# Performance work log

Hardware: AMD Instinct MI355X
Metric: run time of the kernel (lower is better)

## Reference

```python
import jax, jax.numpy as jnp
import numpy as np

K = 20          # neighbors per point
BN_EPS = 1e-5


def setup_inputs() -> dict:
    key = jax.random.key(0)
    k0, k1, k2 = jax.random.split(key, 3)
    B, N, C_OUT, EDGE_DIM = 8, 4096, 64, 4  # edge feat = [diff(3), ||diff||(1)]
    x = jax.random.normal(k0, (B, N, 3), dtype=jnp.float32)
    pos = jax.random.uniform(k1, (B, N, 3), dtype=jnp.float32)
    # shared 1x1-conv MLP params (Conv1d k=1 == per-edge linear) + BatchNorm affine
    W = jax.random.normal(k2, (C_OUT, EDGE_DIM), dtype=jnp.float32) * 0.1
    b = jnp.zeros((C_OUT,), jnp.float32)
    gamma = jnp.ones((C_OUT,), jnp.float32)
    beta = jnp.zeros((C_OUT,), jnp.float32)
    return {"x": x, "pos": pos, "W": W, "b": b, "gamma": gamma, "beta": beta}


def _knn_idx(pos, k):
    # pos: [B, N, 3] -> idx of k nearest neighbors per point, self excluded. [B, N, k]
    B, N, _ = pos.shape
    sq = jnp.sum(pos * pos, axis=-1)                                   # [B, N]
    d2 = sq[:, :, None] + sq[:, None, :] - 2.0 * jnp.einsum('bnd,bmd->bnm', pos, pos)
    d2 = d2 + jnp.eye(N, dtype=pos.dtype) * 1e10                       # exclude self-loop
    _, idx = jax.lax.top_k(-d2, k)                                     # [B, N, k]
    return idx


def _forward(pos, W, b, gamma, beta, k=K):
    idx = _knn_idx(pos, k)                                             # [B, N, k] (int, non-diff)
    nbr = jax.vmap(lambda p, i: p[i])(pos, idx)                        # gather: [B, N, k, 3]
    diff = nbr - pos[:, :, None, :]                                    # neighbor - center
    dist = jnp.sqrt(jnp.sum(diff * diff, axis=-1, keepdims=True))      # [B, N, k, 1]
    feat = jnp.concatenate([diff, dist], axis=-1)                      # [B, N, k, 4]
    # shared MLP (1x1 conv): per-edge linear
    y = jnp.einsum('bnkc,oc->bnko', feat, W) + b                       # [B, N, k, 64]
    # BatchNorm1d over all edges (training-mode batch stats), per channel
    mu = jnp.mean(y, axis=(0, 1, 2))
    var = jnp.var(y, axis=(0, 1, 2))
    y = (y - mu) * jax.lax.rsqrt(var + BN_EPS) * gamma + beta
    y = jax.nn.relu(y)
    y = jnp.where(y >= 0, y, 0.1 * y)   # leaky_relu(0.1) from source (no-op after relu, kept for fidelity)
    return jnp.mean(y, axis=2)          # mean pool over each node's k edges -> [B, N, 64]


def reference(x, pos, W, b, gamma, beta):
    # x only provides (batch_size, num_points) in the source; math uses pos.
    return _forward(pos, W, b, gamma, beta)
```

## Files before the change

kernel.cpp:

```cpp
#include <hip/hip_runtime.h>

#define NB    8
#define NP    4096
#define KNN   20
#define COUT  64
#define S     4
#define BLK   256
#define QPB   (BLK / S)
#define BPB   (NP / QPB)
#define NBLK1 (NB * BPB)
#define NBLK2 ((NB * NP * 4) / BLK)
#define NMOM  14
#define MSTR  16
#define LCAP  32
#define FBIG  3.402823466e38f

typedef unsigned long long u64;
typedef unsigned int u32;

__device__ __forceinline__ void ins20(float d, u32 mi,
                                      float* __restrict__ bd,
                                      u32* __restrict__ bi) {
#pragma unroll
    for (int j = KNN - 1; j >= 1; --j) {
        const bool sh  = d < bd[j - 1];
        const bool in_ = !sh && (d < bd[j]);
        bi[j] = sh ? bi[j - 1] : (in_ ? mi : bi[j]);
        bd[j] = fminf(fmaxf(bd[j - 1], d), bd[j]);
    }
    if (d < bd[0]) { bi[0] = mi; bd[0] = d; }
}

__global__ __launch_bounds__(BLK, 2)
void knn_kernel(const float* __restrict__ pos,
                unsigned short* __restrict__ idx_out,
                float* __restrict__ mom) {
    __shared__ float4 sp[NP];

    const int b = blockIdx.x / BPB;
    const int t = threadIdx.x;
    const int s = t & (S - 1);
    const int n = (blockIdx.x % BPB) * QPB + (t >> 2);
    const float* pb = pos + (size_t)b * NP * 3;

    for (int i = t; i < NP; i += BLK) {
        const float x = pb[3 * i], y = pb[3 * i + 1], z = pb[3 * i + 2];
        const float csq = __fadd_rn(
            __fadd_rn(__fmul_rn(x, x), __fmul_rn(y, y)), __fmul_rn(z, z));
        sp[i] = make_float4(x, y, z, csq);
    }
    __syncthreads();

    const float4 q = sp[n];

    float sd0 = FBIG, sd1 = FBIG, sd2 = FBIG, sd3 = FBIG, sd4 = FBIG;
#pragma unroll 4
    for (int i = 0; i < NP / S; i += 4) {
        const int m = (i << 2) | s;
        const float4 c = sp[m];
        const float dot = fmaf(q.z, c.z, fmaf(q.y, c.y, __fmul_rn(q.x, c.x)));
        const float d2  = __fsub_rn(__fadd_rn(q.w, c.w), __fmul_rn(2.0f, dot));
        if (m != n && d2 < sd4) {
            sd4 = fminf(fmaxf(sd3, d2), sd4);
            sd3 = fminf(fmaxf(sd2, d2), sd3);
            sd2 = fminf(fmaxf(sd1, d2), sd2);
            sd1 = fminf(fmaxf(sd0, d2), sd1);
            sd0 = fminf(sd0, d2);
        }
    }
    float gb = sd4;
    gb = fmaxf(gb, __shfl_xor(gb, 1));
    gb = fmaxf(gb, __shfl_xor(gb, 2));

    float bd[KNN];
    u32   bi[KNN];
#pragma unroll
    for (int j = 0; j < KNN; ++j) { bd[j] = FBIG; bi[j] = 0xFFFu; }
    float p0d = 0.f, p1d = 0.f, p2d = 0.f, p3d = 0.f;
    u32   p0i = 0, p1i = 0, p2i = 0, p3i = 0;
    int   cnt = 0;

#pragma unroll 2
    for (int i = 0; i < NP / S; ++i) {
        const int m = (i << 2) | s;
        const float4 c = sp[m];
        const float dot = fmaf(q.z, c.z, fmaf(q.y, c.y, __fmul_rn(q.x, c.x)));
        const float d2  = __fsub_rn(__fadd_rn(q.w, c.w), __fmul_rn(2.0f, dot));
        const bool acc = (m != n) && (d2 <= gb);
        const bool a0 = acc && (cnt == 0), a1 = acc && (cnt == 1);
        const bool a2 = acc && (cnt == 2), a3 = acc && (cnt == 3);
        p0d = a0 ? d2 : p0d;  p0i = a0 ? (u32)m : p0i;
        p1d = a1 ? d2 : p1d;  p1i = a1 ? (u32)m : p1i;
        p2d = a2 ? d2 : p2d;  p2i = a2 ? (u32)m : p2i;
        p3d = a3 ? d2 : p3d;  p3i = a3 ? (u32)m : p3i;
        cnt += (int)acc;
        if (__ballot(cnt == 4)) {
            ins20(cnt >= 1 ? p0d : FBIG, p0i, bd, bi);
            ins20(cnt >= 2 ? p1d : FBIG, p1i, bd, bi);
            ins20(cnt >= 3 ? p2d : FBIG, p2i, bd, bi);
            ins20(cnt >= 4 ? p3d : FBIG, p3i, bd, bi);
            cnt = 0;
            float g = bd[KNN - 1];
            g = fminf(g, __shfl_xor(g, 1));
            g = fminf(g, __shfl_xor(g, 2));
            gb = fminf(gb, g);
        }
    }
    ins20(cnt >= 1 ? p0d : FBIG, p0i, bd, bi);
    ins20(cnt >= 2 ? p1d : FBIG, p1i, bd, bi);
    ins20(cnt >= 3 ? p2d : FBIG, p2i, bd, bi);
    ins20(cnt >= 4 ? p3d : FBIG, p3i, bd, bi);

    u64 key[LCAP];
#pragma unroll
    for (int j = 0; j < KNN; ++j) {
        u32 fb = __float_as_uint(bd[j]);
        fb ^= (u32)((int)fb >> 31) | 0x80000000u;
        key[j] = ((u64)fb << 12) | bi[j];
    }
#pragma unroll
    for (int j = KNN; j < LCAP; ++j) key[j] = ~0ull;

#pragma unroll
    for (int r = 1; r <= 2; r <<= 1) {
#pragma unroll
        for (int j = 0; j < LCAP / 2; ++j) {
            const int k2 = LCAP - 1 - j;
            const u64 pa = (u64)__shfl_xor((long long)key[k2], r);
            const u64 pc = (u64)__shfl_xor((long long)key[j],  r);
            key[j]  = key[j]  < pa ? key[j]  : pa;
            key[k2] = key[k2] < pc ? key[k2] : pc;
        }
#pragma unroll
        for (int d = 16; d >= 1; d >>= 1) {
#pragma unroll
            for (int j = 0; j < LCAP; ++j) {
                if ((j & d) == 0) {
                    const u64 x = key[j], y = key[j + d];
                    key[j]     = x < y ? x : y;
                    key[j + d] = x < y ? y : x;
                }
            }
        }
    }

    unsigned short* ip = idx_out + ((size_t)b * NP + n) * KNN;
    float s1x = 0, s1y = 0, s1z = 0, s1d = 0;
    float mxx = 0, mxy = 0, mxz = 0, mxd = 0;
    float myy = 0, myz = 0, myd = 0;
    float mzz = 0, mzd = 0, mdd = 0;
#pragma unroll
    for (int j = 0; j < KNN; ++j) {
        const int m = (int)(key[j] & 0xFFFull);
        if ((j & 3) == s) ip[j] = (unsigned short)m;
        const float4 c = sp[m];
        const float dx = __fsub_rn(c.x, q.x);
        const float dy = __fsub_rn(c.y, q.y);
        const float dz = __fsub_rn(c.z, q.z);
        const float dd = sqrtf(__fadd_rn(
            __fadd_rn(__fmul_rn(dx, dx), __fmul_rn(dy, dy)), __fmul_rn(dz, dz)));
        s1x += dx; s1y += dy; s1z += dz; s1d += dd;
        mxx += dx * dx; mxy += dx * dy; mxz += dx * dz; mxd += dx * dd;
        myy += dy * dy; myz += dy * dz; myd += dy * dd;
        mzz += dz * dz; mzd += dz * dd; mdd += dd * dd;
    }
    {
        float vals[NMOM] = {s1x, s1y, s1z, s1d,
                            mxx, mxy, mxz, mxd, myy, myz, myd, mzz, mzd, mdd};
#pragma unroll
        for (int tt = 0; tt < NMOM; ++tt) {
            float v = vals[tt];
#pragma unroll
            for (int off = 32; off > 0; off >>= 1) v += __shfl_down(v, off);
            if ((t & 63) == 0) atomicAdd(&mom[tt * MSTR], v * 0.25f);
        }
    }
}

__global__ __launch_bounds__(BLK)
void out_kernel(const float* __restrict__ pos,
                const float* __restrict__ W,
                const float* __restrict__ bias,
                const float* __restrict__ gamma,
                const float* __restrict__ beta,
                const unsigned short* __restrict__ idx_in,
                const float* __restrict__ mom,
                float* __restrict__ out) {
    __shared__ float sWp[COUT][4];
    __shared__ float sbp[COUT];

    if (threadIdx.x < COUT) {
        const int o = threadIdx.x;
        double S1[4], s2v[10];
#pragma unroll
        for (int tt = 0; tt < 4; ++tt)  S1[tt]  = (double)mom[tt * MSTR];
#pragma unroll
        for (int tt = 0; tt < 10; ++tt) s2v[tt] = (double)mom[(4 + tt) * MSTR];
        const double M = (double)NB * NP * KNN;
        double mean[4];
#pragma unroll
        for (int c = 0; c < 4; ++c) mean[c] = S1[c] / M;
        double E2[4][4];
        E2[0][0] = s2v[0]; E2[0][1] = E2[1][0] = s2v[1];
        E2[0][2] = E2[2][0] = s2v[2]; E2[0][3] = E2[3][0] = s2v[3];
        E2[1][1] = s2v[4]; E2[1][2] = E2[2][1] = s2v[5];
        E2[1][3] = E2[3][1] = s2v[6];
        E2[2][2] = s2v[7]; E2[2][3] = E2[3][2] = s2v[8];
        E2[3][3] = s2v[9];
        double w[4];
#pragma unroll
        for (int c = 0; c < 4; ++c) w[c] = (double)W[o * 4 + c];
        const double bo = (double)bias[o];
        double mu = bo;
#pragma unroll
        for (int c = 0; c < 4; ++c) mu += w[c] * mean[c];
        double var = 0.0;
#pragma unroll
        for (int c = 0; c < 4; ++c)
#pragma unroll
            for (int c2 = 0; c2 < 4; ++c2)
                var += w[c] * w[c2] * (E2[c][c2] / M - mean[c] * mean[c2]);
        const double scale = (double)gamma[o] / sqrt(var + 1e-5);
#pragma unroll
        for (int c = 0; c < 4; ++c) sWp[o][c] = (float)(w[c] * scale);
        sbp[o] = (float)((bo - mu) * scale + (double)beta[o]);
    }
    __syncthreads();

    const int t  = threadIdx.x;
    const int gq = blockIdx.x * (BLK / 4) + (t >> 2);
    const int b  = gq / NP, n = gq % NP;
    const int c0 = (t & 3) * 16;
    const float* pb = pos + (size_t)b * NP * 3;
    const float qx = pb[3 * n], qy = pb[3 * n + 1], qz = pb[3 * n + 2];

    float fx[KNN], fy[KNN], fz[KNN], fd[KNN];
    const unsigned short* ip = idx_in + (size_t)gq * KNN;
#pragma unroll
    for (int j = 0; j < KNN; ++j) {
        const int m = ip[j];
        const float dx = __fsub_rn(pb[3 * m], qx);
        const float dy = __fsub_rn(pb[3 * m + 1], qy);
        const float dz = __fsub_rn(pb[3 * m + 2], qz);
        fx[j] = dx; fy[j] = dy; fz[j] = dz;
        fd[j] = sqrtf(__fadd_rn(
            __fadd_rn(__fmul_rn(dx, dx), __fmul_rn(dy, dy)), __fmul_rn(dz, dz)));
    }

    float* ob = out + (size_t)gq * COUT + c0;
    const float inv = 1.0f / (float)KNN;
#pragma unroll
    for (int o = 0; o < 16; o += 4) {
        float acc[4];
#pragma unroll
        for (int qq = 0; qq < 4; ++qq) {
            const float w0 = sWp[c0 + o + qq][0], w1 = sWp[c0 + o + qq][1];
            const float w2 = sWp[c0 + o + qq][2], w3 = sWp[c0 + o + qq][3];
            const float bb = sbp[c0 + o + qq];
            float a = 0.f;
#pragma unroll
            for (int j = 0; j < KNN; ++j) {
                float y = fmaf(fx[j], w0,
                          fmaf(fy[j], w1, fmaf(fz[j], w2, fmaf(fd[j], w3, bb))));
                a += fmaxf(y, 0.f);
            }
            acc[qq] = a * inv;
        }
        float4 p = {acc[0], acc[1], acc[2], acc[3]};
        *reinterpret_cast<float4*>(ob + o) = p;
    }
}

extern "C" void kernel_launch(void* const* d_in, const int* in_sizes, int n_in,
                              void* d_out, int out_size, void* d_ws, size_t ws_size,
                              hipStream_t stream) {
    (void)in_sizes; (void)n_in; (void)out_size; (void)ws_size;
    const float* pos   = (const float*)d_in[1];
    const float* W     = (const float*)d_in[2];
    const float* bias  = (const float*)d_in[3];
    const float* gamma = (const float*)d_in[4];
    const float* beta  = (const float*)d_in[5];
    float* out = (float*)d_out;

    float* mom = (float*)d_ws;
    unsigned short* idxws = (unsigned short*)((char*)d_ws + 1024);

    hipMemsetAsync(mom, 0, NMOM * MSTR * sizeof(float), stream);
    knn_kernel<<<NBLK1, BLK, 0, stream>>>(pos, idxws, mom);
    out_kernel<<<NBLK2, BLK, 0, stream>>>(pos, W, bias, gamma, beta,
                                          idxws, mom, out);
}
```

Measured before the change: 296.2 us.

## Use tightened speculative KNN threshold with fallback pass and shift-register candidate buffer

The exact-selection pass now starts with a threshold scaled down to 0.58 of the certified 5th-per-lane bound, so fewer candidates pass the filter and fewer 20-element insertions run. If any query in the wave collects fewer than 20 candidates across its 4 lanes, the whole wave redoes the pass with the certified bound. The candidate buffer becomes a shift register guarded by a wave ballot, and the distance uses a fused multiply-add. A wave that needs the fallback pays for a second full scan, and the FMA can change rounding, which may reorder near-tied neighbors.

```diff
diff --git a/kernel.cpp b/kernel.cpp
--- a/kernel.cpp
+++ b/kernel.cpp
@@ -14,6 +14,7 @@
 #define MSTR  16
 #define LCAP  32
 #define FBIG  3.402823466e38f
+#define ALPHA 0.58f
 
 typedef unsigned long long u64;
 typedef unsigned int u32;
@@ -58,8 +59,9 @@
     for (int i = 0; i < NP / S; i += 4) {
         const int m = (i << 2) | s;
         const float4 c = sp[m];
+        const float base = __fadd_rn(q.w, c.w);
         const float dot = fmaf(q.z, c.z, fmaf(q.y, c.y, __fmul_rn(q.x, c.x)));
-        const float d2  = __fsub_rn(__fadd_rn(q.w, c.w), __fmul_rn(2.0f, dot));
+        const float d2  = fmaf(-2.0f, dot, base);
         if (m != n && d2 < sd4) {
             sd4 = fminf(fmaxf(sd3, d2), sd4);
             sd3 = fminf(fmaxf(sd2, d2), sd3);
@@ -68,48 +70,60 @@
             sd0 = fminf(sd0, d2);
         }
     }
-    float gb = sd4;
-    gb = fmaxf(gb, __shfl_xor(gb, 1));
-    gb = fmaxf(gb, __shfl_xor(gb, 2));
+    float gb_cert = sd4;
+    gb_cert = fmaxf(gb_cert, __shfl_xor(gb_cert, 1));
+    gb_cert = fmaxf(gb_cert, __shfl_xor(gb_cert, 2));
 
     float bd[KNN];
     u32   bi[KNN];
-#pragma unroll
-    for (int j = 0; j < KNN; ++j) { bd[j] = FBIG; bi[j] = 0xFFFu; }
-    float p0d = 0.f, p1d = 0.f, p2d = 0.f, p3d = 0.f;
-    u32   p0i = 0, p1i = 0, p2i = 0, p3i = 0;
-    int   cnt = 0;
+    float gbx = ALPHA * gb_cert;
+#pragma unroll 1
+    for (int pass = 0; pass < 2; ++pass) {
+#pragma unroll
+        for (int j = 0; j < KNN; ++j) { bd[j] = FBIG; bi[j] = 0xFFFu; }
+        float p0d = 0.f, p1d = 0.f, p2d = 0.f, p3d = 0.f;
+        u32   p0i = 0, p1i = 0, p2i = 0, p3i = 0;
+        int   cnt = 0, tot = 0;
+        float gb = gbx;
 
 #pragma unroll 2
-    for (int i = 0; i < NP / S; ++i) {
-        const int m = (i << 2) | s;
-        const float4 c = sp[m];
-        const float dot = fmaf(q.z, c.z, fmaf(q.y, c.y, __fmul_rn(q.x, c.x)));
-        const float d2  = __fsub_rn(__fadd_rn(q.w, c.w), __fmul_rn(2.0f, dot));
-        const bool acc = (m != n) && (d2 <= gb);
-        const bool a0 = acc && (cnt == 0), a1 = acc && (cnt == 1);
-        const bool a2 = acc && (cnt == 2), a3 = acc && (cnt == 3);
-        p0d = a0 ? d2 : p0d;  p0i = a0 ? (u32)m : p0i;
-        p1d = a1 ? d2 : p1d;  p1i = a1 ? (u32)m : p1i;
-        p2d = a2 ? d2 : p2d;  p2i = a2 ? (u32)m : p2i;
-        p3d = a3 ? d2 : p3d;  p3i = a3 ? (u32)m : p3i;
-        cnt += (int)acc;
-        if (__ballot(cnt == 4)) {
-            ins20(cnt >= 1 ? p0d : FBIG, p0i, bd, bi);
-            ins20(cnt >= 2 ? p1d : FBIG, p1i, bd, bi);
-            ins20(cnt >= 3 ? p2d : FBIG, p2i, bd, bi);
-            ins20(cnt >= 4 ? p3d : FBIG, p3i, bd, bi);
-            cnt = 0;
-            float g = bd[KNN - 1];
-            g = fminf(g, __shfl_xor(g, 1));
-            g = fminf(g, __shfl_xor(g, 2));
-            gb = fminf(gb, g);
-        }
-    }
-    ins20(cnt >= 1 ? p0d : FBIG, p0i, bd, bi);
-    ins20(cnt >= 2 ? p1d : FBIG, p1i, bd, bi);
-    ins20(cnt >= 3 ? p2d : FBIG, p2i, bd, bi);
-    ins20(cnt >= 4 ? p3d : FBIG, p3i, bd, bi);
+        for (int i = 0; i < NP / S; ++i) {
+            const int m = (i << 2) | s;
+            const float4 c = sp[m];
+            const float base = __fadd_rn(q.w, c.w);
+            const float dot = fmaf(q.z, c.z, fmaf(q.y, c.y, __fmul_rn(q.x, c.x)));
+            const float d2  = fmaf(-2.0f, dot, base);
+            const bool acc = (m != n) && (d2 <= gb);
+            if (__ballot(acc)) {
+                p3d = acc ? p2d : p3d;  p3i = acc ? p2i : p3i;
+                p2d = acc ? p1d : p2d;  p2i = acc ? p1i : p2i;
+                p1d = acc ? p0d : p1d;  p1i = acc ? p0i : p1i;
+                p0d = acc ? d2  : p0d;  p0i = acc ? (u32)m : p0i;
+                cnt += (int)acc;  tot += (int)acc;
+                if (__ballot(cnt == 4)) {
+                    ins20(cnt >= 4 ? p3d : FBIG, p3i, bd, bi);
+                    ins20(cnt >= 3 ? p2d : FBIG, p2i, bd, bi);
+                    ins20(cnt >= 2 ? p1d : FBIG, p1i, bd, bi);
+                    ins20(cnt >= 1 ? p0d : FBIG, p0i, bd, bi);
+                    cnt = 0;
+                    float g = bd[KNN - 1];
+                    g = fminf(g, __shfl_xor(g, 1));
+                    g = fminf(g, __shfl_xor(g, 2));
+                    gb = fminf(gb, g);
+                }
+            }
+        }
+        ins20(cnt >= 4 ? p3d : FBIG, p3i, bd, bi);
+        ins20(cnt >= 3 ? p2d : FBIG, p2i, bd, bi);
+        ins20(cnt >= 2 ? p1d : FBIG, p1i, bd, bi);
+        ins20(cnt >= 1 ? p0d : FBIG, p0i, bd, bi);
+
+        int gt = tot;
+        gt += __shfl_xor(gt, 1);
+        gt += __shfl_xor(gt, 2);
+        if (__ballot(gt < 20) == 0ull) break;
+        gbx = gb_cert;
+    }
 
     u64 key[LCAP];
 #pragma unroll
```

Result: slower. 347.6 us (+17.4%).
